# Kernel tuning notes

Hardware: AMD Instinct MI355X
Metric: run time of the kernel (lower is better)

## Reference

```python
import jax, jax.numpy as jnp
import numpy as np

B, T, D, H = 2, 2048, 2048, 16
HS = D // H  # head size 128


def setup_inputs() -> dict:
    key = jax.random.key(0)
    ks = jax.random.split(key, 5)
    s = 0.02
    return {
        "x": jax.random.normal(ks[0], (B, T, D), dtype=jnp.float32),
        "wq": jax.random.normal(ks[1], (D, D), dtype=jnp.float32) * s,
        "wk": jax.random.normal(ks[2], (D, D), dtype=jnp.float32) * s,
        "wv": jax.random.normal(ks[3], (D, D), dtype=jnp.float32) * s,
        "wo": jax.random.normal(ks[4], (D, D), dtype=jnp.float32) * s,
    }


def reference(x, wq, wk, wv, wo):
    b, t, d = x.shape
    # projections: nn.Linear(x) = x @ W.T ; here W stored as (out,in)
    q = (x @ wq.T).reshape(b, t, H, HS).transpose(0, 2, 1, 3)  # (B,H,T,HS)
    k = (x @ wk.T).reshape(b, t, H, HS).transpose(0, 2, 1, 3)
    v = (x @ wv.T).reshape(b, t, H, HS).transpose(0, 2, 1, 3)
    scale = 1.0 / np.sqrt(HS).astype(np.float32)
    e = jnp.einsum("bhqd,bhkd->bhqk", q, k) * scale  # (B,H,T,T)
    causal = jnp.tril(jnp.ones((t, t), dtype=bool))
    e = jnp.where(causal[None, None], e, jnp.float32(-jnp.inf))
    alpha = jax.nn.softmax(e, axis=-1)  # dropout=0.0 -> identity
    attn = jnp.einsum("bhqk,bhkd->bhqd", alpha, v)
    attn = attn.transpose(0, 2, 1, 3).reshape(b, t, d)
    return attn @ wo.T
```

## Files before the change

kernel.cpp:

```cpp
#include <hip/hip_runtime.h>
#include <hip/hip_bf16.h>

typedef __bf16 bf16x8 __attribute__((ext_vector_type(8)));
typedef float f32x4 __attribute__((ext_vector_type(4)));
typedef unsigned short u16x8 __attribute__((ext_vector_type(8)));

#define GLDS16(g, s)                                                         \
  __builtin_amdgcn_global_load_lds(                                          \
      (const __attribute__((address_space(1))) void*)(g),                    \
      (__attribute__((address_space(3))) void*)(s), 16, 0, 0)

__device__ __forceinline__ void store1(__hip_bfloat16* p, float v) { *p = __float2bfloat16(v); }
__device__ __forceinline__ void store1(float* p, float v) { *p = v; }

__global__ __launch_bounds__(256) void cast_f32_to_bf16(const float4* __restrict__ in,
                                                        ushort4* __restrict__ out, int n4) {
  int i = blockIdx.x * 256 + threadIdx.x;
  if (i >= n4) return;
  float4 v = in[i];
  union { ushort4 u; __hip_bfloat16 h[4]; } o;
  o.h[0] = __float2bfloat16(v.x);
  o.h[1] = __float2bfloat16(v.y);
  o.h[2] = __float2bfloat16(v.z);
  o.h[3] = __float2bfloat16(v.w);
  out[i] = o.u;
}

__global__ __launch_bounds__(256) void cast4_f32_to_bf16(const float4* __restrict__ w0,
                                                         const float4* __restrict__ w1,
                                                         const float4* __restrict__ w2,
                                                         const float4* __restrict__ w3,
                                                         ushort4* __restrict__ o0,
                                                         ushort4* __restrict__ o1,
                                                         ushort4* __restrict__ o2,
                                                         ushort4* __restrict__ o3, int n4) {
  int i = blockIdx.x * 256 + threadIdx.x;
  if (i >= n4) return;
  int s = blockIdx.y;
  const float4* in = (s == 0) ? w0 : (s == 1) ? w1 : (s == 2) ? w2 : w3;
  ushort4* out = (s == 0) ? o0 : (s == 1) ? o1 : (s == 2) ? o2 : o3;
  float4 v = in[i];
  union { ushort4 u; __hip_bfloat16 h[4]; } o;
  o.h[0] = __float2bfloat16(v.x);
  o.h[1] = __float2bfloat16(v.y);
  o.h[2] = __float2bfloat16(v.z);
  o.h[3] = __float2bfloat16(v.w);
  out[i] = o.u;
}

__global__ __launch_bounds__(512, 2) void gemm_qkv3(const __hip_bfloat16* __restrict__ A,
                                                    const __hip_bfloat16* __restrict__ B0,
                                                    const __hip_bfloat16* __restrict__ B1,
                                                    const __hip_bfloat16* __restrict__ B2,
                                                    __hip_bfloat16* __restrict__ C0,
                                                    __hip_bfloat16* __restrict__ C1,
                                                    __hip_bfloat16* __restrict__ C2,
                                                    int nBx, int nBy, int N, int K) {
  __shared__ __hip_bfloat16 As[2][128 * 64];
  __shared__ __hip_bfloat16 Bs[2][3][128 * 64];

  const int t = threadIdx.x;
  const int w = t >> 6, l = t & 63;
  const int lr = l & 15, hi = l >> 4;

  const int nwg = nBx * nBy;
  int id = (int)blockIdx.x;
  id = (id & 7) * (nwg >> 3) + (id >> 3);
  const int bx = id / nBy;
  const int by = id % nBy;

  const int n0 = bx * 128;
  const int m0 = by * 128;

  const int c0r = t >> 3, cs = t & 7;
  const int c1r = 64 + c0r;
  const size_t aoff0 = (size_t)(m0 + c0r) * K + (cs ^ (c0r & 7)) * 8;
  const size_t aoff1 = (size_t)(m0 + c1r) * K + (cs ^ (c1r & 7)) * 8;
  const size_t boff0 = (size_t)(n0 + c0r) * K + (cs ^ (c0r & 7)) * 8;
  const size_t boff1 = (size_t)(n0 + c1r) * K + (cs ^ (c1r & 7)) * 8;

#define STAGE_T(bb, koff)                                                    \
  do {                                                                       \
    GLDS16(A + aoff0 + (koff), (char*)As[bb] + t * 16);                      \
    GLDS16(A + aoff1 + (koff), (char*)As[bb] + 8192 + t * 16);               \
    GLDS16(B0 + boff0 + (koff), (char*)Bs[bb][0] + t * 16);                  \
    GLDS16(B0 + boff1 + (koff), (char*)Bs[bb][0] + 8192 + t * 16);           \
    GLDS16(B1 + boff0 + (koff), (char*)Bs[bb][1] + t * 16);                  \
    GLDS16(B1 + boff1 + (koff), (char*)Bs[bb][1] + 8192 + t * 16);           \
    GLDS16(B2 + boff0 + (koff), (char*)Bs[bb][2] + t * 16);                  \
    GLDS16(B2 + boff1 + (koff), (char*)Bs[bb][2] + 8192 + t * 16);           \
  } while (0)

  f32x4 acc[3][4][2] = {};
  bf16x8 af[4][2];
  const int NT = K / 64;
  const int sw = lr & 7;
  const int arow = (w >> 2) * 64;
  const int brow = (w & 3) * 32;

#define WAITV(n)  asm volatile("s_waitcnt vmcnt(" #n ")" ::: "memory")

  STAGE_T(0, 0);

  for (int tt = 0; tt < NT; ++tt) {
    const int buf = tt & 1, nb = buf ^ 1;
    const bool stg = (tt + 1 < NT);
    const size_t ko = (size_t)(tt + 1) * 64;

    WAITV(0);
    __builtin_amdgcn_s_barrier();

#pragma unroll
    for (int mi = 0; mi < 4; ++mi)
#pragma unroll
      for (int kk = 0; kk < 2; ++kk)
        af[mi][kk] = *(const bf16x8*)((const char*)As[buf] +
            (arow + mi * 16 + lr) * 128 + (((kk * 4 + hi) ^ sw) << 4));

    if (stg) STAGE_T(nb, ko);

#pragma unroll
    for (int m = 0; m < 3; ++m) {
      bf16x8 bq[2][2];
#pragma unroll
      for (int ni = 0; ni < 2; ++ni)
#pragma unroll
        for (int kk = 0; kk < 2; ++kk)
          bq[ni][kk] = *(const bf16x8*)((const char*)Bs[buf][m] +
              (brow + ni * 16 + lr) * 128 + (((kk * 4 + hi) ^ sw) << 4));
      __builtin_amdgcn_s_setprio(1);
#pragma unroll
      for (int mi = 0; mi < 4; ++mi)
#pragma unroll
        for (int ni = 0; ni < 2; ++ni) {
          acc[m][mi][ni] = __builtin_amdgcn_mfma_f32_16x16x32_bf16(
              af[mi][0], bq[ni][0], acc[m][mi][ni], 0, 0, 0);
          acc[m][mi][ni] = __builtin_amdgcn_mfma_f32_16x16x32_bf16(
              af[mi][1], bq[ni][1], acc[m][mi][ni], 0, 0, 0);
        }
      __builtin_amdgcn_s_setprio(0);
    }
  }
#undef WAITV
#undef STAGE_T

#pragma unroll
  for (int m = 0; m < 3; ++m) {
    __hip_bfloat16* Cm = (m == 0) ? C0 : (m == 1) ? C1 : C2;
#pragma unroll
    for (int mi = 0; mi < 4; ++mi)
#pragma unroll
      for (int ni = 0; ni < 2; ++ni)
#pragma unroll
        for (int i = 0; i < 4; ++i) {
          size_t idx = (size_t)(m0 + arow + mi * 16 + hi * 4 + i) * N +
                       (n0 + brow + ni * 16 + lr);
          store1(&Cm[idx], acc[m][mi][ni][i]);
        }
  }
}

template <typename OutT>
__global__ __launch_bounds__(512, 2) void gemm256(const __hip_bfloat16* __restrict__ A,
                                                  const __hip_bfloat16* __restrict__ B0,
                                                  OutT* __restrict__ C0,
                                                  int nBx, int nBy, int N, int K) {
  __shared__ __hip_bfloat16 As[2][128 * 64];
  __shared__ __hip_bfloat16 Bs[2][256 * 64];

  const int t = threadIdx.x;
  const int w = t >> 6, l = t & 63;
  const int lr = l & 15, hi = l >> 4;

  const int nwg = nBx * nBy;
  int id = (int)blockIdx.x;
  id = (id & 7) * (nwg >> 3) + (id >> 3);
  const int bx = id / nBy;
  const int by = id % nBy;

  const int n0 = bx * 256;
  const int m0 = by * 128;

  const int c0r = t >> 3, cs = t & 7;
  const int c1r = 64 + c0r;
  const __hip_bfloat16* aP0 = A + (size_t)(m0 + c0r) * K + (cs ^ (c0r & 7)) * 8;
  const __hip_bfloat16* aP1 = A + (size_t)(m0 + c1r) * K + (cs ^ (c1r & 7)) * 8;
  const __hip_bfloat16* bP0 = B0 + (size_t)(n0 + c0r) * K + (cs ^ (c0r & 7)) * 8;
  const __hip_bfloat16* bP1 = B0 + (size_t)(n0 + c1r) * K + (cs ^ (c1r & 7)) * 8;
  const size_t HK = (size_t)128 * K;

#define STAGE_T(bb, koff)                                                    \
  do {                                                                       \
    GLDS16(aP0 + (koff), (char*)As[bb] + t * 16);                            \
    GLDS16(aP1 + (koff), (char*)As[bb] + 8192 + t * 16);                     \
    GLDS16(bP0 + (koff), (char*)Bs[bb] + t * 16);                            \
    GLDS16(bP1 + (koff), (char*)Bs[bb] + 8192 + t * 16);                     \
    GLDS16(bP0 + HK + (koff), (char*)Bs[bb] + 16384 + t * 16);               \
    GLDS16(bP1 + HK + (koff), (char*)Bs[bb] + 24576 + t * 16);               \
  } while (0)

  f32x4 acc[2][4][2] = {};
  bf16x8 afA[4][2];
  bf16x8 bqA[2][2], bqB[2][2];
  const int NT = K / 64;
  const int sw = lr & 7;
  const int arow = (w >> 2) * 64;
  const int brow = (w & 3) * 32;

#define RD_A(dst)                                                            \
  _Pragma("unroll") for (int mi = 0; mi < 4; ++mi)                           \
    _Pragma("unroll") for (int kk = 0; kk < 2; ++kk)                         \
      dst[mi][kk] = *(const bf16x8*)((const char*)As[buf] +                  \
          (arow + mi * 16 + lr) * 128 + (((kk * 4 + hi) ^ sw) << 4));
#define RD_B(dst, nh)                                                        \
  _Pragma("unroll") for (int ni = 0; ni < 2; ++ni)                           \
    _Pragma("unroll") for (int kk = 0; kk < 2; ++kk)                         \
      dst[ni][kk] = *(const bf16x8*)((const char*)Bs[buf] +                  \
          ((nh) * 128 + brow + ni * 16 + lr) * 128 + (((kk * 4 + hi) ^ sw) << 4));
#define MFMA_Q(nh, afv, bq)                                                  \
  do {                                                                       \
    __builtin_amdgcn_s_setprio(1);                                           \
    _Pragma("unroll") for (int mi = 0; mi < 4; ++mi)                         \
      _Pragma("unroll") for (int ni = 0; ni < 2; ++ni) {                     \
        acc[nh][mi][ni] = __builtin_amdgcn_mfma_f32_16x16x32_bf16(           \
            afv[mi][0], bq[ni][0], acc[nh][mi][ni], 0, 0, 0);                \
        acc[nh][mi][ni] = __builtin_amdgcn_mfma_f32_16x16x32_bf16(           \
            afv[mi][1], bq[ni][1], acc[nh][mi][ni], 0, 0, 0);                \
      }                                                                      \
    __builtin_amdgcn_s_setprio(0);                                           \
  } while (0)
#define WAITV(n)  asm volatile("s_waitcnt vmcnt(" #n ")" ::: "memory")

  STAGE_T(0, 0);

  for (int tt = 0; tt < NT; ++tt) {
    const int buf = tt & 1, nb = buf ^ 1;
    const bool stg = (tt + 1 < NT);
    const size_t ko = (size_t)(tt + 1) * 64;

    WAITV(0);
    __builtin_amdgcn_s_barrier();
    RD_A(afA);
    RD_B(bqA, 0);
    RD_B(bqB, 1);
    if (stg) STAGE_T(nb, ko);
    MFMA_Q(0, afA, bqA);
    MFMA_Q(1, afA, bqB);
  }
#undef WAITV
#undef MFMA_Q
#undef RD_B
#undef RD_A
#undef STAGE_T

#pragma unroll
  for (int nh = 0; nh < 2; ++nh)
#pragma unroll
    for (int mi = 0; mi < 4; ++mi)
#pragma unroll
      for (int ni = 0; ni < 2; ++ni)
#pragma unroll
        for (int i = 0; i < 4; ++i) {
          size_t idx = (size_t)(m0 + arow + mi * 16 + hi * 4 + i) * N +
                       (n0 + nh * 128 + brow + ni * 16 + lr);
          store1(&C0[idx], acc[nh][mi][ni][i]);
        }
}

__global__ __launch_bounds__(256, 2) void flash_attn(const __hip_bfloat16* __restrict__ Qg,
                                                     const __hip_bfloat16* __restrict__ Kg,
                                                     const __hip_bfloat16* __restrict__ Vg,
                                                     __hip_bfloat16* __restrict__ Og) {
  __shared__ __hip_bfloat16 Ks[2][64 * 128];
  __shared__ __hip_bfloat16 Vt[128 * 64];

  const int mblk = blockIdx.x;
  const int bh = mblk & 31;
  const int jj = mblk >> 5;
  const int qt = (jj < 8) ? (15 - jj) : (jj - 8);
  const int b = bh >> 4, h = bh & 15;
  const int q0 = qt * 128;
  const int t = threadIdx.x, w = t >> 6, l = t & 63;
  const int lr = l & 15, hi = l >> 4;
  const size_t base = ((size_t)b * 2048) * 2048 + (size_t)h * 128;
  const int nt = 2 * qt + 2;
  const float scale = 0.08838834764831843f;

  const int hi2 = (hi & 1) * 2;
  const int addrA = (((hi2) << 4) | lr) << 2;
  const int addrB = (((hi2 + 1) << 4) | lr) << 2;
  int addr_o[4];
#pragma unroll
  for (int i = 0; i < 4; ++i) addr_o[i] = ((l & 48) | (hi * 4 + i)) << 2;
  const bool hiHigh = (hi >> 1) != 0;

  bf16x8 qf[2][4];
#pragma unroll
  for (int g = 0; g < 2; ++g) {
    const __hip_bfloat16* qrow = Qg + base + (size_t)(q0 + w * 32 + g * 16 + lr) * 2048;
#pragma unroll
    for (int kk = 0; kk < 4; ++kk)
      qf[g][kk] = *(const bf16x8*)(qrow + kk * 32 + hi * 8);
  }

  f32x4 o_acc[2][8] = {};
  float m_run[2] = {-1e30f, -1e30f};
  float l_run[2] = {0.f, 0.f};

  const __hip_bfloat16* kptr[4];
#pragma unroll
  for (int i = 0; i < 4; ++i) {
    int c = i * 256 + t;
    int kr = c >> 4;
    int ke = ((c & 15) ^ (kr & 7)) * 8;
    kptr[i] = Kg + base + (size_t)kr * 2048 + ke;
  }
  const __hip_bfloat16* vptr[2];
#pragma unroll
  for (int it = 0; it < 2; ++it) {
    int kp = it * 16 + w * 4 + hi;
    vptr[it] = Vg + base + (size_t)(kp * 2) * 2048 + lr * 8;
  }

  u16x8 va[2], vb[2];
#pragma unroll
  for (int i = 0; i < 4; ++i)
    GLDS16(kptr[i], (char*)Ks[0] + (i * 256 + t) * 16);
#pragma unroll
  for (int it = 0; it < 2; ++it) {
    va[it] = *(const u16x8*)vptr[it];
    vb[it] = *(const u16x8*)(vptr[it] + 2048);
  }

  for (int kt = 0; kt < nt; ++kt) {
    const int cur = kt & 1;
    const int kb = kt * 64;
    __syncthreads();

#pragma unroll
    for (int it = 0; it < 2; ++it)
#pragma unroll
      for (int j2 = 0; j2 < 8; ++j2) {
        int d = lr * 8 + j2;
        int sw = (lr ^ j2) & 7;
        int off = d * 128 + (((it * 4 + w) ^ sw) << 4) + hi * 4;
        *(unsigned int*)((char*)Vt + off) =
            (unsigned int)va[it][j2] | ((unsigned int)vb[it][j2] << 16);
      }
    if (kt + 1 < nt) {
      const size_t adv = (size_t)(kb + 64) * 2048;
#pragma unroll
      for (int i = 0; i < 4; ++i)
        GLDS16(kptr[i] + adv, (char*)Ks[cur ^ 1] + (i * 256 + t) * 16);
#pragma unroll
      for (int it = 0; it < 2; ++it) {
        va[it] = *(const u16x8*)(vptr[it] + adv);
        vb[it] = *(const u16x8*)(vptr[it] + adv + 2048);
      }
    }
    asm volatile("s_waitcnt lgkmcnt(0)" ::: "memory");
    __builtin_amdgcn_s_barrier();

    if (!(kt == nt - 1 && w < 2)) {
      const char* ks = (const char*)Ks[cur];

      f32x4 st[2][4];
#pragma unroll
      for (int g = 0; g < 2; ++g)
#pragma unroll
        for (int nk = 0; nk < 4; ++nk) { f32x4 z = {}; st[g][nk] = z; }
#pragma unroll
      for (int nk = 0; nk < 4; ++nk)
#pragma unroll
        for (int kk = 0; kk < 4; ++kk) {
          bf16x8 kf = *(const bf16x8*)(ks + (nk * 16 + lr) * 256 +
                                       (((kk * 4 + hi) ^ (lr & 7)) << 4));
#pragma unroll
          for (int g = 0; g < 2; ++g)
            st[g][nk] = __builtin_amdgcn_mfma_f32_16x16x32_bf16(kf, qf[g][kk], st[g][nk], 0, 0, 0);
        }

      const bool maskt = (kt >= nt - 2);
#pragma unroll
      for (int g = 0; g < 2; ++g)
#pragma unroll
        for (int nk = 0; nk < 4; ++nk)
#pragma unroll
          for (int i = 0; i < 4; ++i) {
            float v = st[g][nk][i] * scale;
            if (maskt) {
              int ki = kb + nk * 16 + hi * 4 + i;
              int qi = q0 + w * 32 + g * 16 + lr;
              if (ki > qi) v = -1e30f;
            }
            st[g][nk][i] = v;
          }

      bf16x8 paf[2][2];
#pragma unroll
      for (int g = 0; g < 2; ++g) {
        float t0 = fmaxf(fmaxf(st[g][0][0], st[g][0][1]), fmaxf(st[g][0][2], st[g][0][3]));
        float t1 = fmaxf(fmaxf(st[g][1][0], st[g][1][1]), fmaxf(st[g][1][2], st[g][1][3]));
        float t2 = fmaxf(fmaxf(st[g][2][0], st[g][2][1]), fmaxf(st[g][2][2], st[g][2][3]));
        float t3 = fmaxf(fmaxf(st[g][3][0], st[g][3][1]), fmaxf(st[g][3][2], st[g][3][3]));
        float mx = fmaxf(fmaxf(t0, t1), fmaxf(t2, t3));
        mx = fmaxf(mx, __shfl_xor(mx, 16));
        mx = fmaxf(mx, __shfl_xor(mx, 32));

        if (!__all(mx - m_run[g] <= 8.0f)) {
          float mnew = fmaxf(m_run[g], mx);
          float rs = __expf(m_run[g] - mnew);
          m_run[g] = mnew;
          l_run[g] *= rs;
          int rsi = __float_as_int(rs);
#pragma unroll
          for (int i = 0; i < 4; ++i) {
            float rso = __int_as_float(__builtin_amdgcn_ds_bpermute(addr_o[i], rsi));
#pragma unroll
            for (int nc = 0; nc < 8; ++nc) o_acc[g][nc][i] *= rso;
          }
        }

#pragma unroll
        for (int nk = 0; nk < 4; ++nk)
#pragma unroll
          for (int i = 0; i < 4; ++i)
            st[g][nk][i] = __expf(st[g][nk][i] - m_run[g]);

        float s0 = (st[g][0][0] + st[g][0][1]) + (st[g][0][2] + st[g][0][3]);
        float s1 = (st[g][1][0] + st[g][1][1]) + (st[g][1][2] + st[g][1][3]);
        float s2 = (st[g][2][0] + st[g][2][1]) + (st[g][2][2] + st[g][2][3]);
        float s3 = (st[g][3][0] + st[g][3][1]) + (st[g][3][2] + st[g][3][3]);
        float sm = (s0 + s1) + (s2 + s3);
        sm += __shfl_xor(sm, 16);
        sm += __shfl_xor(sm, 32);
        l_run[g] += sm;

        unsigned pk[4][2];
#pragma unroll
        for (int nk = 0; nk < 4; ++nk) {
          asm("v_cvt_pk_bf16_f32 %0, %1, %2"
              : "=v"(pk[nk][0]) : "v"(st[g][nk][0]), "v"(st[g][nk][1]));
          asm("v_cvt_pk_bf16_f32 %0, %1, %2"
              : "=v"(pk[nk][1]) : "v"(st[g][nk][2]), "v"(st[g][nk][3]));
        }

#pragma unroll
        for (int kk = 0; kk < 2; ++kk) {
          unsigned au[4];
#pragma unroll
          for (int p = 0; p < 4; ++p) {
            int ad = (p < 2) ? addrA : addrB;
            int v0 = __builtin_amdgcn_ds_bpermute(ad, (int)pk[2 * kk][p & 1]);
            int v1 = __builtin_amdgcn_ds_bpermute(ad, (int)pk[2 * kk + 1][p & 1]);
            au[p] = hiHigh ? (unsigned)v1 : (unsigned)v0;
          }
          union { unsigned u[4]; bf16x8 v; } cv;
          cv.u[0] = au[0]; cv.u[1] = au[1]; cv.u[2] = au[2]; cv.u[3] = au[3];
          paf[g][kk] = cv.v;
        }
      }

#pragma unroll
      for (int kk = 0; kk < 2; ++kk)
#pragma unroll
        for (int nc = 0; nc < 8; ++nc) {
          int d = nc * 16 + lr;
          int sw = ((d >> 3) ^ d) & 7;
          bf16x8 vfr = *(const bf16x8*)((const char*)Vt + d * 128 +
                                        (((kk * 4 + hi) ^ sw) << 4));
#pragma unroll
          for (int g = 0; g < 2; ++g)
            o_acc[g][nc] = __builtin_amdgcn_mfma_f32_16x16x32_bf16(paf[g][kk], vfr, o_acc[g][nc], 0, 0, 0);
        }
    }
  }

#pragma unroll
  for (int g = 0; g < 2; ++g) {
    float lo[4];
#pragma unroll
    for (int i = 0; i < 4; ++i)
      lo[i] = __int_as_float(__builtin_amdgcn_ds_bpermute(addr_o[i], __float_as_int(l_run[g])));
#pragma unroll
    for (int nc = 0; nc < 8; ++nc)
#pragma unroll
      for (int i = 0; i < 4; ++i) {
        float val = o_acc[g][nc][i] / lo[i];
        Og[base + (size_t)(q0 + w * 32 + g * 16 + hi * 4 + i) * 2048 + nc * 16 + lr] =
            __float2bfloat16(val);
      }
  }
}

extern "C" void kernel_launch(void* const* d_in, const int* in_sizes, int n_in,
                              void* d_out, int out_size, void* d_ws, size_t ws_size,
                              hipStream_t stream) {
  const float* x  = (const float*)d_in[0];
  const float* wq = (const float*)d_in[1];
  const float* wk = (const float*)d_in[2];
  const float* wv = (const float*)d_in[3];
  const float* wo = (const float*)d_in[4];
  float* out = (float*)d_out;

  const int BT = 4096, D = 2048;
  const size_t ND = (size_t)D * D;
  const size_t NX = (size_t)BT * D;

  __hip_bfloat16* xb  = (__hip_bfloat16*)d_ws;
  __hip_bfloat16* wqb = xb + NX;
  __hip_bfloat16* wkb = wqb + ND;
  __hip_bfloat16* wvb = wkb + ND;
  __hip_bfloat16* wob = wvb + ND;
  __hip_bfloat16* Qb  = wob + ND;
  __hip_bfloat16* Kb  = Qb + NX;
  __hip_bfloat16* Vb  = Kb + NX;
  __hip_bfloat16* Ab  = Vb + NX;

  cast_f32_to_bf16<<<(int)(NX / 4 / 256), 256, 0, stream>>>((const float4*)x, (ushort4*)xb, (int)(NX / 4));
  cast4_f32_to_bf16<<<dim3((int)(ND / 4 / 256), 4), 256, 0, stream>>>(
      (const float4*)wq, (const float4*)wk, (const float4*)wv, (const float4*)wo,
      (ushort4*)wqb, (ushort4*)wkb, (ushort4*)wvb, (ushort4*)wob, (int)(ND / 4));

  gemm_qkv3<<<512, 512, 0, stream>>>(xb, wqb, wkb, wvb, Qb, Kb, Vb, 16, 32, D, D);

  flash_attn<<<512, 256, 0, stream>>>(Qb, Kb, Vb, Ab);

  gemm256<float><<<256, 512, 0, stream>>>(Ab, wob, out, 8, 32, D, D);
}
```

Baseline: 274.6 us.

## Split QKV GEMM into per-matrix 128x256 tiles with triple-buffered K=32 pipeline

The fused QKV projection kernel, which used to compute all three weight matrices for a 128x128 output tile, now has each workgroup compute a single 128x256 tile of one matrix, selected by block index, over 768 workgroups. The K loop switches from a 64-wide double buffer to a 32-wide triple buffer that prefetches two stages ahead with a partial vmcnt wait. This cuts the accumulator count and LDS footprint and improves load/compute overlap. The cost is that each x tile is loaded separately for every matrix instead of being shared across Q, K and V.

After: 269.6 us (median of 2 runs). No clear change (-1.8%).

```diff
diff --git a/kernel.cpp b/kernel.cpp
--- a/kernel.cpp
+++ b/kernel.cpp
@@ -48,16 +48,17 @@
   out[i] = o.u;
 }
 
-__global__ __launch_bounds__(512, 2) void gemm_qkv3(const __hip_bfloat16* __restrict__ A,
-                                                    const __hip_bfloat16* __restrict__ B0,
-                                                    const __hip_bfloat16* __restrict__ B1,
-                                                    const __hip_bfloat16* __restrict__ B2,
-                                                    __hip_bfloat16* __restrict__ C0,
-                                                    __hip_bfloat16* __restrict__ C1,
-                                                    __hip_bfloat16* __restrict__ C2,
-                                                    int nBx, int nBy, int N, int K) {
-  __shared__ __hip_bfloat16 As[2][128 * 64];
-  __shared__ __hip_bfloat16 Bs[2][3][128 * 64];
+__global__ __launch_bounds__(512, 2) void gemm_qkv(const __hip_bfloat16* __restrict__ A,
+                                                   const __hip_bfloat16* __restrict__ B0,
+                                                   const __hip_bfloat16* __restrict__ B1,
+                                                   const __hip_bfloat16* __restrict__ B2,
+                                                   __hip_bfloat16* __restrict__ C0,
+                                                   __hip_bfloat16* __restrict__ C1,
+                                                   __hip_bfloat16* __restrict__ C2,
+                                                   int nBx, int nBy, int ntPerMat,
+                                                   int N, int K) {
+  __shared__ __hip_bfloat16 As[3][128 * 32];
+  __shared__ __hip_bfloat16 Bs[3][256 * 32];
 
   const int t = threadIdx.x;
   const int w = t >> 6, l = t & 63;
@@ -69,84 +70,73 @@
   const int bx = id / nBy;
   const int by = id % nBy;
 
-  const int n0 = bx * 128;
+  const int sel = bx / ntPerMat;
+  const __hip_bfloat16* Bm = (sel == 0) ? B0 : ((sel == 1) ? B1 : B2);
+  __hip_bfloat16* Cm = (sel == 0) ? C0 : ((sel == 1) ? C1 : C2);
+  const int n0 = (bx - sel * ntPerMat) * 256;
   const int m0 = by * 128;
 
-  const int c0r = t >> 3, cs = t & 7;
-  const int c1r = 64 + c0r;
-  const size_t aoff0 = (size_t)(m0 + c0r) * K + (cs ^ (c0r & 7)) * 8;
-  const size_t aoff1 = (size_t)(m0 + c1r) * K + (cs ^ (c1r & 7)) * 8;
-  const size_t boff0 = (size_t)(n0 + c0r) * K + (cs ^ (c0r & 7)) * 8;
-  const size_t boff1 = (size_t)(n0 + c1r) * K + (cs ^ (c1r & 7)) * 8;
+  const int ar = t >> 2, as_ = t & 3;
+  const int swsrc = (as_ ^ ((ar >> 1) & 3)) * 8;
+  const __hip_bfloat16* aP  = A  + (size_t)(m0 + ar) * K + swsrc;
+  const __hip_bfloat16* bPa = Bm + (size_t)(n0 + ar) * K + swsrc;
+  const __hip_bfloat16* bPb = Bm + (size_t)(n0 + 128 + ar) * K + swsrc;
 
 #define STAGE_T(bb, koff)                                                    \
   do {                                                                       \
-    GLDS16(A + aoff0 + (koff), (char*)As[bb] + t * 16);                      \
-    GLDS16(A + aoff1 + (koff), (char*)As[bb] + 8192 + t * 16);               \
-    GLDS16(B0 + boff0 + (koff), (char*)Bs[bb][0] + t * 16);                  \
-    GLDS16(B0 + boff1 + (koff), (char*)Bs[bb][0] + 8192 + t * 16);           \
-    GLDS16(B1 + boff0 + (koff), (char*)Bs[bb][1] + t * 16);                  \
-    GLDS16(B1 + boff1 + (koff), (char*)Bs[bb][1] + 8192 + t * 16);           \
-    GLDS16(B2 + boff0 + (koff), (char*)Bs[bb][2] + t * 16);                  \
-    GLDS16(B2 + boff1 + (koff), (char*)Bs[bb][2] + 8192 + t * 16);           \
+    GLDS16(aP + (koff), (char*)As[bb] + t * 16);                             \
+    GLDS16(bPa + (koff), (char*)Bs[bb] + t * 16);                            \
+    GLDS16(bPb + (koff), (char*)Bs[bb] + 8192 + t * 16);                     \
   } while (0)
 
-  f32x4 acc[3][4][2] = {};
-  bf16x8 af[4][2];
-  const int NT = K / 64;
-  const int sw = lr & 7;
+  f32x4 acc[2][4][2] = {};
+  bf16x8 af[4];
+  bf16x8 bq[2][2];
+  const int NT = K / 32;
+  const int swr = (lr >> 1) & 3;
   const int arow = (w >> 2) * 64;
   const int brow = (w & 3) * 32;
 
 #define WAITV(n)  asm volatile("s_waitcnt vmcnt(" #n ")" ::: "memory")
 
   STAGE_T(0, 0);
+  STAGE_T(1, 32);
 
   for (int tt = 0; tt < NT; ++tt) {
-    const int buf = tt & 1, nb = buf ^ 1;
-    const bool stg = (tt + 1 < NT);
-    const size_t ko = (size_t)(tt + 1) * 64;
-
-    WAITV(0);
+    const int buf = tt % 3;
+
+    if (tt + 1 < NT) WAITV(3); else WAITV(0);
     __builtin_amdgcn_s_barrier();
 
 #pragma unroll
     for (int mi = 0; mi < 4; ++mi)
-#pragma unroll
-      for (int kk = 0; kk < 2; ++kk)
-        af[mi][kk] = *(const bf16x8*)((const char*)As[buf] +
-            (arow + mi * 16 + lr) * 128 + (((kk * 4 + hi) ^ sw) << 4));
-
-    if (stg) STAGE_T(nb, ko);
-
-#pragma unroll
-    for (int m = 0; m < 3; ++m) {
-      bf16x8 bq[2][2];
+      af[mi] = *(const bf16x8*)((const char*)As[buf] +
+          (arow + mi * 16 + lr) * 64 + ((hi ^ swr) << 4));
+#pragma unroll
+    for (int nh = 0; nh < 2; ++nh)
 #pragma unroll
       for (int ni = 0; ni < 2; ++ni)
-#pragma unroll
-        for (int kk = 0; kk < 2; ++kk)
-          bq[ni][kk] = *(const bf16x8*)((const char*)Bs[buf][m] +
-              (brow + ni * 16 + lr) * 128 + (((kk * 4 + hi) ^ sw) << 4));
-      __builtin_amdgcn_s_setprio(1);
+        bq[nh][ni] = *(const bf16x8*)((const char*)Bs[buf] +
+            (nh * 128 + brow + ni * 16 + lr) * 64 + ((hi ^ swr) << 4));
+
+    if (tt + 2 < NT) STAGE_T((tt + 2) % 3, (size_t)(tt + 2) * 32);
+
+    __builtin_amdgcn_s_setprio(1);
+#pragma unroll
+    for (int nh = 0; nh < 2; ++nh)
 #pragma unroll
       for (int mi = 0; mi < 4; ++mi)
 #pragma unroll
-        for (int ni = 0; ni < 2; ++ni) {
-          acc[m][mi][ni] = __builtin_amdgcn_mfma_f32_16x16x32_bf16(
-              af[mi][0], bq[ni][0], acc[m][mi][ni], 0, 0, 0);
-          acc[m][mi][ni] = __builtin_amdgcn_mfma_f32_16x16x32_bf16(
-              af[mi][1], bq[ni][1], acc[m][mi][ni], 0, 0, 0);
-        }
-      __builtin_amdgcn_s_setprio(0);
-    }
+        for (int ni = 0; ni < 2; ++ni)
+          acc[nh][mi][ni] = __builtin_amdgcn_mfma_f32_16x16x32_bf16(
+              af[mi], bq[nh][ni], acc[nh][mi][ni], 0, 0, 0);
+    __builtin_amdgcn_s_setprio(0);
   }
 #undef WAITV
 #undef STAGE_T
 
 #pragma unroll
-  for (int m = 0; m < 3; ++m) {
-    __hip_bfloat16* Cm = (m == 0) ? C0 : (m == 1) ? C1 : C2;
+  for (int nh = 0; nh < 2; ++nh)
 #pragma unroll
     for (int mi = 0; mi < 4; ++mi)
 #pragma unroll
@@ -154,14 +144,13 @@
 #pragma unroll
         for (int i = 0; i < 4; ++i) {
           size_t idx = (size_t)(m0 + arow + mi * 16 + hi * 4 + i) * N +
-                       (n0 + brow + ni * 16 + lr);
-          store1(&Cm[idx], acc[m][mi][ni][i]);
-        }
-  }
+                       (n0 + nh * 128 + brow + ni * 16 + lr);
+          store1(&Cm[idx], acc[nh][mi][ni][i]);
+        }
 }
 
 template <typename OutT>
-__global__ __launch_bounds__(512, 2) void gemm256(const __hip_bfloat16* __restrict__ A,
+__global__ __launch_bounds__(512, 2) void gemm_op(const __hip_bfloat16* __restrict__ A,
                                                   const __hip_bfloat16* __restrict__ B0,
                                                   OutT* __restrict__ C0,
                                                   int nBx, int nBy, int N, int K) {
@@ -522,9 +511,10 @@
       (const float4*)wq, (const float4*)wk, (const float4*)wv, (const float4*)wo,
       (ushort4*)wqb, (ushort4*)wkb, (ushort4*)wvb, (ushort4*)wob, (int)(ND / 4));
 
-  gemm_qkv3<<<512, 512, 0, stream>>>(xb, wqb, wkb, wvb, Qb, Kb, Vb, 16, 32, D, D);
+  gemm_qkv<<<768, 512, 0, stream>>>(
+      xb, wqb, wkb, wvb, Qb, Kb, Vb, 24, 32, 8, D, D);
 
   flash_attn<<<512, 256, 0, stream>>>(Qb, Kb, Vb, Ab);
 
-  gemm256<float><<<256, 512, 0, stream>>>(Ab, wob, out, 8, 32, D, D);
+  gemm_op<float><<<256, 512, 0, stream>>>(Ab, wob, out, 8, 32, D, D);
 }
```
